# Kernel optimization log

Measured on AMD Instinct MI355X. Metric: run time of the kernel, lower is better.

The kernel has to match this reference:

```python
import jax, jax.numpy as jnp
import numpy as np

N_NODES = 100000
N_EDGES = 3200000
F_IN = 256
HID = 64
N_CLS = 16


def setup_inputs() -> dict:
    key = jax.random.key(0)
    ks = jax.random.split(key, 12)
    x = jax.random.normal(ks[0], (N_NODES, F_IN), dtype=jnp.float32)
    edge_index = jax.random.randint(ks[1], (2, N_EDGES), 0, N_NODES, dtype=jnp.int32)
    w_mul = jax.random.normal(ks[2], (N_EDGES, 1), dtype=jnp.float32)
    s1 = 1.0 / np.sqrt(F_IN)
    s2 = 1.0 / np.sqrt(HID)
    # layer 1 params
    lin1_w = jax.random.uniform(ks[3], (HID, F_IN), minval=-s1, maxval=s1, dtype=jnp.float32)
    lin1_b = jax.random.uniform(ks[4], (HID,), minval=-s1, maxval=s1, dtype=jnp.float32)
    mlp1_w0 = jax.random.uniform(ks[5], (HID, 1), minval=-1.0, maxval=1.0, dtype=jnp.float32)
    mlp1_w1 = jax.random.uniform(ks[6], (HID, HID), minval=-s2, maxval=s2, dtype=jnp.float32)
    mlp1_b1 = jax.random.uniform(ks[7], (HID,), minval=-s2, maxval=s2, dtype=jnp.float32)
    # layer 2 params
    lin2_w = jax.random.uniform(ks[8], (N_CLS, HID), minval=-s2, maxval=s2, dtype=jnp.float32)
    lin2_b = jax.random.uniform(ks[9], (N_CLS,), minval=-s2, maxval=s2, dtype=jnp.float32)
    mlp2_w0 = jax.random.uniform(ks[10], (HID, 1), minval=-1.0, maxval=1.0, dtype=jnp.float32)
    mlp2_w1 = jax.random.uniform(ks[11], (N_CLS, HID), minval=-s2, maxval=s2, dtype=jnp.float32)
    mlp2_b1 = jnp.zeros((N_CLS,), dtype=jnp.float32)
    return dict(x=x, edge_index=edge_index, w_mul=w_mul,
                lin1_w=lin1_w, lin1_b=lin1_b, mlp1_w0=mlp1_w0, mlp1_w1=mlp1_w1, mlp1_b1=mlp1_b1,
                lin2_w=lin2_w, lin2_b=lin2_b, mlp2_w0=mlp2_w0, mlp2_w1=mlp2_w1, mlp2_b1=mlp2_b1)


def curv_layer(x, src, dst, w_mul, lin_w, lin_b, m_w0, m_w1, m_b1, n_nodes):
    # dense projection: [N, out]
    h = x @ lin_w.T + lin_b
    # per-edge weight MLP: Linear(1,HID,no bias) -> LeakyReLU(0.2) -> Linear(HID,out,bias)
    ew = jax.nn.leaky_relu(w_mul @ m_w0.T, negative_slope=0.2) @ m_w1.T + m_b1  # [E, out]
    # segment softmax keyed by source node (PyG softmax(out_weight, edge_index[0]))
    emax = jax.ops.segment_max(ew, src, num_segments=n_nodes)  # [N, out]
    e = jnp.exp(ew - emax[src])
    esum = jax.ops.segment_sum(e, src, num_segments=n_nodes)
    alpha = e / (esum[src] + 1e-16)  # [E, out]
    # message = alpha * x_j (x_j = h[src]); scatter-add at destination
    msg = alpha * h[src]
    return jax.ops.segment_sum(msg, dst, num_segments=n_nodes)  # [N, out]


def reference(x, edge_index, w_mul,
              lin1_w, lin1_b, mlp1_w0, mlp1_w1, mlp1_b1,
              lin2_w, lin2_b, mlp2_w0, mlp2_w1, mlp2_b1):
    src, dst = edge_index[0], edge_index[1]
    n = x.shape[0]
    # eval mode: dropout(p=0.8) is identity
    h = curv_layer(x, src, dst, w_mul, lin1_w, lin1_b, mlp1_w0, mlp1_w1, mlp1_b1, n)
    h = jax.nn.elu(h)
    h = curv_layer(h, src, dst, w_mul, lin2_w, lin2_b, mlp2_w0, mlp2_w1, mlp2_b1, n)
    return jax.nn.log_softmax(h, axis=1)
```

## Files before the change

kernel.cpp:

```cpp
#include <hip/hip_runtime.h>
#include <math.h>

#define FIN 256
#define HID 64
#define NCLS 16
#define BSH 8
#define BWD (1 << BSH)
#define NBKMAX 512
#define CAP 9216
#define CHUNK_S 16384
#define CHUNK_D 8192

__global__ __launch_bounds__(512) void init_kernel(int* gcur_s, int* gcur_d) {
    int tid = threadIdx.x;
    gcur_s[tid] = tid * CAP;
    gcur_d[tid] = tid * CAP;
}

__global__ __launch_bounds__(512) void stage_kernel(const int* __restrict__ ei,
                                                    const float* __restrict__ w,
                                                    int* gcur_s, int* gcur_d,
                                                    unsigned int* st_s, uint2* st_d,
                                                    int E, int nchunk_s) {
    __shared__ int lh[NBKMAX];
    __shared__ int lofs[NBKMAX];
    __shared__ int lcur[NBKMAX];
    __shared__ int gbase[NBKMAX];
    __shared__ uint2 buf2[CHUNK_D];
    unsigned int* buf1 = (unsigned int*)buf2;
    int tid = threadIdx.x;
    int side = (blockIdx.x >= nchunk_s) ? 1 : 0;
    lh[tid] = 0;
    __syncthreads();
    if (!side) {
        int base = blockIdx.x * CHUNK_S;
        #pragma unroll
        for (int j = 0; j < CHUNK_S / 512; j++) {
            int e = base + tid + j * 512;
            if (e < E) atomicAdd(&lh[((unsigned)ei[e]) >> BSH], 1);
        }
    } else {
        int base = (blockIdx.x - nchunk_s) * CHUNK_D;
        #pragma unroll
        for (int j = 0; j < CHUNK_D / 512; j++) {
            int e = base + tid + j * 512;
            if (e < E) atomicAdd(&lh[((unsigned)ei[E + e]) >> BSH], 1);
        }
    }
    __syncthreads();
    int v = lh[tid];
    lofs[tid] = v;
    __syncthreads();
    for (int off = 1; off < 512; off <<= 1) {
        int add = (tid >= off) ? lofs[tid - off] : 0;
        __syncthreads();
        lofs[tid] += add;
        __syncthreads();
    }
    int ex = lofs[tid] - v;
    lofs[tid] = ex;
    lcur[tid] = ex;
    __syncthreads();
    if (!side) {
        int base = blockIdx.x * CHUNK_S;
        #pragma unroll
        for (int j = 0; j < CHUNK_S / 512; j++) {
            int e = base + tid + j * 512;
            if (e < E) {
                int s = ei[e];
                unsigned int rec = (__float_as_uint(w[e]) & 0xFFFFFF00u) | (unsigned int)(s & 0xFF);
                int p = atomicAdd(&lcur[((unsigned)s) >> BSH], 1);
                buf1[p] = rec;
            }
        }
    } else {
        int base = (blockIdx.x - nchunk_s) * CHUNK_D;
        #pragma unroll
        for (int j = 0; j < CHUNK_D / 512; j++) {
            int e = base + tid + j * 512;
            if (e < E) {
                int d = ei[E + e];
                int s = ei[e];
                unsigned int rec = (__float_as_uint(w[e]) & 0xFFFFFF00u) | (unsigned int)(d & 0xFF);
                int p = atomicAdd(&lcur[((unsigned)d) >> BSH], 1);
                buf2[p] = make_uint2((unsigned int)s, rec);
            }
        }
    }
    __syncthreads();
    {
        int c = lh[tid];
        if (c) gbase[tid] = atomicAdd(side ? &gcur_d[tid] : &gcur_s[tid], c);
    }
    __syncthreads();
    int wv = tid >> 6, lane = tid & 63;
    if (!side) {
        for (int b = wv; b < NBKMAX; b += 8) {
            int c = lh[b];
            int ls = lofs[b], gs = gbase[b];
            for (int i = lane; i < c; i += 64) st_s[gs + i] = buf1[ls + i];
        }
    } else {
        for (int b = wv; b < NBKMAX; b += 8) {
            int c = lh[b];
            int ls = lofs[b], gs = gbase[b];
            for (int i = lane; i < c; i += 64) st_d[gs + i] = buf2[ls + i];
        }
    }
}

__global__ __launch_bounds__(512) void bucket_scan_kernel(const int* gcur_s, const int* gcur_d,
                                                          int* bbase_s, int* bbase_d,
                                                          int* offs_s, int* offs_d,
                                                          int N, int nbk, int E) {
    int side = blockIdx.x;
    const int* gc = side ? gcur_d : gcur_s;
    int* bb = side ? bbase_d : bbase_s;
    __shared__ int tmp[512];
    int tid = threadIdx.x;
    int v = (tid < nbk) ? (gc[tid] - tid * CAP) : 0;
    tmp[tid] = v;
    __syncthreads();
    for (int off = 1; off < 512; off <<= 1) {
        int add = (tid >= off) ? tmp[tid - off] : 0;
        __syncthreads();
        tmp[tid] += add;
        __syncthreads();
    }
    if (tid < nbk) bb[tid] = tmp[tid] - v;
    if (tid == 0) {
        bb[nbk] = E;
        (side ? offs_d : offs_s)[N] = E;
    }
}

__global__ __launch_bounds__(256) void bucket_build_s_kernel(const int* __restrict__ bbase,
                                                             const unsigned int* __restrict__ st,
                                                             int* offs, float* t_s, int N) {
    int b = blockIdx.x;
    int r0 = bbase[b];
    int cnt = bbase[b + 1] - r0;
    if (cnt > CAP) cnt = CAP;
    size_t sb = (size_t)b * CAP;
    int n0 = b << BSH;
    int nn = min(BWD, N - n0);
    __shared__ int lh[BWD];
    __shared__ int lofs[BWD];
    __shared__ float buf[CAP];
    int tid = threadIdx.x;
    lh[tid] = 0;
    __syncthreads();
    for (int i = tid; i < cnt; i += 256) atomicAdd(&lh[st[sb + i] & 0xFFu], 1);
    __syncthreads();
    int v = lh[tid];
    lofs[tid] = v;
    __syncthreads();
    for (int off = 1; off < 256; off <<= 1) {
        int add = (tid >= off) ? lofs[tid - off] : 0;
        __syncthreads();
        lofs[tid] += add;
        __syncthreads();
    }
    int ex = lofs[tid] - v;
    if (tid < nn) offs[n0 + tid] = r0 + ex;
    lofs[tid] = ex;
    __syncthreads();
    for (int i = tid; i < cnt; i += 256) {
        unsigned int rec = st[sb + i];
        int p = atomicAdd(&lofs[rec & 0xFFu], 1);
        buf[p] = __uint_as_float(rec & 0xFFFFFF00u);
    }
    __syncthreads();
    for (int i = tid; i < cnt; i += 256) t_s[r0 + i] = buf[i];
}

__global__ __launch_bounds__(256) void bucket_build_d_kernel(const int* __restrict__ bbase,
                                                             const uint2* __restrict__ st,
                                                             int* offs, int2* ed, int N) {
    int b = blockIdx.x;
    int r0 = bbase[b];
    int cnt = bbase[b + 1] - r0;
    if (cnt > CAP) cnt = CAP;
    size_t sb = (size_t)b * CAP;
    int n0 = b << BSH;
    int nn = min(BWD, N - n0);
    __shared__ int lh[BWD];
    __shared__ int lofs[BWD];
    __shared__ int2 buf[CAP];
    int tid = threadIdx.x;
    lh[tid] = 0;
    __syncthreads();
    for (int i = tid; i < cnt; i += 256) atomicAdd(&lh[st[sb + i].y & 0xFFu], 1);
    __syncthreads();
    int v = lh[tid];
    lofs[tid] = v;
    __syncthreads();
    for (int off = 1; off < 256; off <<= 1) {
        int add = (tid >= off) ? lofs[tid - off] : 0;
        __syncthreads();
        lofs[tid] += add;
        __syncthreads();
    }
    int ex = lofs[tid] - v;
    if (tid < nn) offs[n0 + tid] = r0 + ex;
    lofs[tid] = ex;
    __syncthreads();
    for (int i = tid; i < cnt; i += 256) {
        uint2 rec = st[sb + i];
        int p = atomicAdd(&lofs[rec.y & 0xFFu], 1);
        buf[p] = make_int2((int)rec.x, (int)(rec.y & 0xFFFFFF00u));
    }
    __syncthreads();
    for (int i = tid; i < cnt; i += 256) ed[r0 + i] = buf[i];
}

__global__ void prep_kernel(const float* __restrict__ w0a, const float* __restrict__ w1a,
                            const float* __restrict__ w0b, const float* __restrict__ w1b,
                            float* Ap1, float* An1, float* Ap2, float* An2) {
    int tid = threadIdx.x;
    if (tid < 64) {
        float ap = 0.f, an = 0.f;
        for (int j = 0; j < 64; j++) {
            float w0 = w0a[j];
            float w1 = w1a[tid * 64 + j];
            ap += w0 * ((w0 >= 0.f) ? 1.f : 0.2f) * w1;
            an += w0 * ((w0 <= 0.f) ? 1.f : 0.2f) * w1;
        }
        Ap1[tid] = ap; An1[tid] = an;
    } else if (tid < 80) {
        int k = tid - 64;
        float ap = 0.f, an = 0.f;
        for (int j = 0; j < 64; j++) {
            float w0 = w0b[j];
            float w1 = w1b[k * 64 + j];
            ap += w0 * ((w0 >= 0.f) ? 1.f : 0.2f) * w1;
            an += w0 * ((w0 <= 0.f) ? 1.f : 0.2f) * w1;
        }
        Ap2[k] = ap; An2[k] = an;
    }
}

__global__ __launch_bounds__(256) void esum1_kernel(const int* __restrict__ offs,
                                                    const float* __restrict__ t_s,
                                                    const float* __restrict__ Ap,
                                                    const float* __restrict__ An,
                                                    float* __restrict__ inv, int N) {
    int node = blockIdx.x * 4 + (threadIdx.x >> 6);
    int k = threadIdx.x & 63;
    if (node >= N) return;
    int s0 = offs[node], s1 = offs[node + 1];
    float ap = Ap[k], an = An[k];
    float sum = 0.f;
    int i = s0;
    for (; i + 3 < s1; i += 4) {
        float t0 = t_s[i], t1 = t_s[i + 1], t2 = t_s[i + 2], t3 = t_s[i + 3];
        sum += __expf(t0 * ((t0 >= 0.f) ? ap : an));
        sum += __expf(t1 * ((t1 >= 0.f) ? ap : an));
        sum += __expf(t2 * ((t2 >= 0.f) ? ap : an));
        sum += __expf(t3 * ((t3 >= 0.f) ? ap : an));
    }
    for (; i < s1; i++) {
        float t = t_s[i];
        sum += __expf(t * ((t >= 0.f) ? ap : an));
    }
    inv[(size_t)node * 64 + k] = (s1 > s0) ? 1.f / (sum + 1e-16f) : 0.f;
}

__global__ __launch_bounds__(256) void esum2_kernel(const int* __restrict__ offs,
                                                    const float* __restrict__ t_s,
                                                    const float* __restrict__ Ap,
                                                    const float* __restrict__ An,
                                                    float* __restrict__ inv, int N) {
    int node = blockIdx.x * 16 + (threadIdx.x >> 4);
    int k = threadIdx.x & 15;
    if (node >= N) return;
    int s0 = offs[node], s1 = offs[node + 1];
    float ap = Ap[k], an = An[k];
    float sum = 0.f;
    int i = s0;
    for (; i + 3 < s1; i += 4) {
        float t0 = t_s[i], t1 = t_s[i + 1], t2 = t_s[i + 2], t3 = t_s[i + 3];
        sum += __expf(t0 * ((t0 >= 0.f) ? ap : an));
        sum += __expf(t1 * ((t1 >= 0.f) ? ap : an));
        sum += __expf(t2 * ((t2 >= 0.f) ? ap : an));
        sum += __expf(t3 * ((t3 >= 0.f) ? ap : an));
    }
    for (; i < s1; i++) {
        float t = t_s[i];
        sum += __expf(t * ((t >= 0.f) ? ap : an));
    }
    inv[(size_t)node * 16 + k] = (s1 > s0) ? 1.f / (sum + 1e-16f) : 0.f;
}

__device__ __forceinline__ unsigned int bf16rn(float f) {
    unsigned int u = __float_as_uint(f);
    return (u + 0x7fffu + ((u >> 16) & 1u)) >> 16;
}

#define GP 68
__global__ __launch_bounds__(256) void gemm1_kernel(const float* __restrict__ x,
                                                    const float* __restrict__ W,
                                                    const float* __restrict__ b,
                                                    const float* __restrict__ inv,
                                                    uint2* __restrict__ g1, int N) {
    __shared__ float xs[32][GP];
    __shared__ float wsh[32][GP];
    int block_row = blockIdx.x * 64;
    int tid = threadIdx.x;
    int tr = tid / 16, tc = tid % 16;
    float acc[4][4] = {{0.f}};
    for (int k0 = 0; k0 < FIN; k0 += 32) {
        #pragma unroll
        for (int i = 0; i < 2; i++) {
            int idx = tid + i * 256;
            int r = idx >> 3;
            int c4 = idx & 7;
            int gr = block_row + r;
            float4 v = (gr < N) ? *(const float4*)&x[(size_t)gr * FIN + k0 + c4 * 4]
                                : make_float4(0.f, 0.f, 0.f, 0.f);
            xs[c4 * 4 + 0][r] = v.x; xs[c4 * 4 + 1][r] = v.y;
            xs[c4 * 4 + 2][r] = v.z; xs[c4 * 4 + 3][r] = v.w;
            float4 wv = *(const float4*)&W[r * FIN + k0 + c4 * 4];
            wsh[c4 * 4 + 0][r] = wv.x; wsh[c4 * 4 + 1][r] = wv.y;
            wsh[c4 * 4 + 2][r] = wv.z; wsh[c4 * 4 + 3][r] = wv.w;
        }
        __syncthreads();
        #pragma unroll
        for (int kk = 0; kk < 32; kk++) {
            float4 xv = *(const float4*)&xs[kk][tr * 4];
            float4 wv = *(const float4*)&wsh[kk][tc * 4];
            acc[0][0] += xv.x * wv.x; acc[0][1] += xv.x * wv.y; acc[0][2] += xv.x * wv.z; acc[0][3] += xv.x * wv.w;
            acc[1][0] += xv.y * wv.x; acc[1][1] += xv.y * wv.y; acc[1][2] += xv.y * wv.z; acc[1][3] += xv.y * wv.w;
            acc[2][0] += xv.z * wv.x; acc[2][1] += xv.z * wv.y; acc[2][2] += xv.z * wv.z; acc[2][3] += xv.z * wv.w;
            acc[3][0] += xv.w * wv.x; acc[3][1] += xv.w * wv.y; acc[3][2] += xv.w * wv.z; acc[3][3] += xv.w * wv.w;
        }
        __syncthreads();
    }
    float4 bv = ((const float4*)b)[tc];
    #pragma unroll
    for (int i = 0; i < 4; i++) {
        int gr = block_row + tr * 4 + i;
        if (gr < N) {
            float4 iv = *(const float4*)&inv[(size_t)gr * 64 + tc * 4];
            float o0 = (acc[i][0] + bv.x) * iv.x;
            float o1 = (acc[i][1] + bv.y) * iv.y;
            float o2 = (acc[i][2] + bv.z) * iv.z;
            float o3 = (acc[i][3] + bv.w) * iv.w;
            uint2 p;
            p.x = bf16rn(o0) | (bf16rn(o1) << 16);
            p.y = bf16rn(o2) | (bf16rn(o3) << 16);
            g1[(size_t)gr * 16 + tc] = p;
        }
    }
}

__global__ __launch_bounds__(256) void gemm2_kernel(const float* __restrict__ x2,
                                                    const float* __restrict__ W2,
                                                    const float* __restrict__ b2,
                                                    const float* __restrict__ inv,
                                                    float* __restrict__ g2, int N) {
    __shared__ float ws[16][GP];
    __shared__ float xs[16][GP];
    __shared__ float bs[16];
    int tid = threadIdx.x;
    {
        int c = tid >> 4, j4 = tid & 15;
        float4 v = ((const float4*)W2)[tid];
        ws[c][j4 * 4 + 0] = v.x; ws[c][j4 * 4 + 1] = v.y;
        ws[c][j4 * 4 + 2] = v.z; ws[c][j4 * 4 + 3] = v.w;
    }
    if (tid < 16) bs[tid] = b2[tid];
    int node0 = blockIdx.x * 16;
    {
        int r = tid >> 4, c4 = tid & 15;
        int gn = node0 + r;
        float4 v = (gn < N) ? *(const float4*)&x2[(size_t)gn * 64 + c4 * 4]
                            : make_float4(0.f, 0.f, 0.f, 0.f);
        xs[r][c4 * 4 + 0] = v.x; xs[r][c4 * 4 + 1] = v.y;
        xs[r][c4 * 4 + 2] = v.z; xs[r][c4 * 4 + 3] = v.w;
    }
    __syncthreads();
    int node_l = tid >> 4, col = tid & 15;
    int gn = node0 + node_l;
    if (gn >= N) return;
    float acc = bs[col];
    #pragma unroll
    for (int j4 = 0; j4 < 16; j4++) {
        float4 xv = *(const float4*)&xs[node_l][j4 * 4];
        float4 wv = *(const float4*)&ws[col][j4 * 4];
        acc += xv.x * wv.x + xv.y * wv.y + xv.z * wv.z + xv.w * wv.w;
    }
    g2[(size_t)gn * NCLS + col] = acc * inv[(size_t)gn * NCLS + col];
}

__global__ __launch_bounds__(256) void agg1_kernel(const int* __restrict__ offs,
                                                   const int2* __restrict__ ed,
                                                   const float* __restrict__ Ap,
                                                   const float* __restrict__ An,
                                                   const uint2* __restrict__ g,
                                                   float* __restrict__ x2, int N) {
    int node = blockIdx.x * 16 + (threadIdx.x >> 4);
    int l = threadIdx.x & 15;
    if (node >= N) return;
    int d0 = offs[node], d1 = offs[node + 1];
    float4 ap = ((const float4*)Ap)[l];
    float4 an = ((const float4*)An)[l];
    float4 acc = make_float4(0.f, 0.f, 0.f, 0.f);
    int i = d0;
    int end8 = d0 + ((d1 - d0) & ~7);
    for (; i < end8; i += 8) {
        int2 e[8];
        #pragma unroll
        for (int j = 0; j < 8; j++) e[j] = ed[i + j];
        uint2 gv[8];
        #pragma unroll
        for (int j = 0; j < 8; j++)
            gv[j] = g[((size_t)e[j].x << 4) + l];
        #pragma unroll
        for (int j = 0; j < 8; j++) {
            float t = __int_as_float(e[j].y);
            float4 a = (t >= 0.f) ? ap : an;
            float ex = __expf(t * a.x), ey = __expf(t * a.y);
            float ez = __expf(t * a.z), ew = __expf(t * a.w);
            acc.x += ex * __uint_as_float(gv[j].x << 16);
            acc.y += ey * __uint_as_float(gv[j].x & 0xffff0000u);
            acc.z += ez * __uint_as_float(gv[j].y << 16);
            acc.w += ew * __uint_as_float(gv[j].y & 0xffff0000u);
        }
    }
    for (; i < d1; i++) {
        int2 e = ed[i];
        float t = __int_as_float(e.y);
        float4 a = (t >= 0.f) ? ap : an;
        uint2 gv = g[((size_t)e.x << 4) + l];
        acc.x += __expf(t * a.x) * __uint_as_float(gv.x << 16);
        acc.y += __expf(t * a.y) * __uint_as_float(gv.x & 0xffff0000u);
        acc.z += __expf(t * a.z) * __uint_as_float(gv.y << 16);
        acc.w += __expf(t * a.w) * __uint_as_float(gv.y & 0xffff0000u);
    }
    float4 o;
    o.x = (acc.x > 0.f) ? acc.x : (__expf(acc.x) - 1.f);
    o.y = (acc.y > 0.f) ? acc.y : (__expf(acc.y) - 1.f);
    o.z = (acc.z > 0.f) ? acc.z : (__expf(acc.z) - 1.f);
    o.w = (acc.w > 0.f) ? acc.w : (__expf(acc.w) - 1.f);
    *(float4*)(x2 + ((size_t)node << 6) + l * 4) = o;
}

__global__ __launch_bounds__(256) void agg2_kernel(const int* __restrict__ offs,
                                                   const int2* __restrict__ ed,
                                                   const float* __restrict__ Ap,
                                                   const float* __restrict__ An,
                                                   const float* __restrict__ g,
                                                   float* __restrict__ out, int N) {
    int node = blockIdx.x * 64 + (threadIdx.x >> 2);
    int l = threadIdx.x & 3;
    if (node >= N) return;
    int d0 = offs[node], d1 = offs[node + 1];
    float4 ap = ((const float4*)Ap)[l];
    float4 an = ((const float4*)An)[l];
    float4 acc = make_float4(0.f, 0.f, 0.f, 0.f);
    int i = d0;
    int end8 = d0 + ((d1 - d0) & ~7);
    for (; i < end8; i += 8) {
        int2 e[8];
        #pragma unroll
        for (int j = 0; j < 8; j++) e[j] = ed[i + j];
        float4 gv[8];
        #pragma unroll
        for (int j = 0; j < 8; j++)
            gv[j] = *(const float4*)(g + ((size_t)e[j].x << 4) + l * 4);
        #pragma unroll
        for (int j = 0; j < 8; j++) {
            float t = __int_as_float(e[j].y);
            float4 a = (t >= 0.f) ? ap : an;
            acc.x += __expf(t * a.x) * gv[j].x;
            acc.y += __expf(t * a.y) * gv[j].y;
            acc.z += __expf(t * a.z) * gv[j].z;
            acc.w += __expf(t * a.w) * gv[j].w;
        }
    }
    for (; i < d1; i++) {
        int2 e = ed[i];
        float t = __int_as_float(e.y);
        float4 a = (t >= 0.f) ? ap : an;
        float4 gv = *(const float4*)(g + ((size_t)e.x << 4) + l * 4);
        acc.x += __expf(t * a.x) * gv.x;
        acc.y += __expf(t * a.y) * gv.y;
        acc.z += __expf(t * a.z) * gv.z;
        acc.w += __expf(t * a.w) * gv.w;
    }
    float m = fmaxf(fmaxf(acc.x, acc.y), fmaxf(acc.z, acc.w));
    m = fmaxf(m, __shfl_xor(m, 1, 4));
    m = fmaxf(m, __shfl_xor(m, 2, 4));
    float s = __expf(acc.x - m) + __expf(acc.y - m) + __expf(acc.z - m) + __expf(acc.w - m);
    s += __shfl_xor(s, 1, 4);
    s += __shfl_xor(s, 2, 4);
    float lse = m + __logf(s);
    float4 o = make_float4(acc.x - lse, acc.y - lse, acc.z - lse, acc.w - lse);
    *(float4*)(out + ((size_t)node << 4) + l * 4) = o;
}

extern "C" void kernel_launch(void* const* d_in, const int* in_sizes, int n_in,
                              void* d_out, int out_size, void* d_ws, size_t ws_size,
                              hipStream_t stream) {
    const float* x      = (const float*)d_in[0];
    const int*   ei     = (const int*)d_in[1];
    const float* wmul   = (const float*)d_in[2];
    const float* lin1_w = (const float*)d_in[3];
    const float* lin1_b = (const float*)d_in[4];
    const float* m1w0   = (const float*)d_in[5];
    const float* m1w1   = (const float*)d_in[6];
    const float* lin2_w = (const float*)d_in[8];
    const float* lin2_b = (const float*)d_in[9];
    const float* m2w0   = (const float*)d_in[10];
    const float* m2w1   = (const float*)d_in[11];

    int N = in_sizes[0] / FIN;
    int E = in_sizes[1] / 2;
    int nbk = (N + BWD - 1) >> BSH;
    int nchunk_s = (E + CHUNK_S - 1) / CHUNK_S;
    int nchunk_d = (E + CHUNK_D - 1) / CHUNK_D;

    char* ws = (char*)d_ws;
    auto alloc = [&](size_t bytes) {
        char* p = ws;
        ws += (bytes + 255) & ~(size_t)255;
        return p;
    };
    int*   gcur_s  = (int*)alloc(NBKMAX * 4);
    int*   gcur_d  = (int*)alloc(NBKMAX * 4);
    int*   bbase_s = (int*)alloc((NBKMAX + 1) * 4);
    int*   bbase_d = (int*)alloc((NBKMAX + 1) * 4);
    float* Ap1     = (float*)alloc(64 * 4);
    float* An1     = (float*)alloc(64 * 4);
    float* Ap2     = (float*)alloc(16 * 4);
    float* An2     = (float*)alloc(16 * 4);
    int*   offs_s  = (int*)alloc((size_t)(N + 1) * 4);
    int*   offs_d  = (int*)alloc((size_t)(N + 1) * 4);
    float* t_s     = (float*)alloc((size_t)E * 4);
    int2*  ed      = (int2*)alloc((size_t)E * 8);
    char*  reg = ws;
    unsigned int* st_s = (unsigned int*)(reg);
    uint2*        st_d = (uint2*)(reg + (((size_t)nbk * CAP * 4 + 255) & ~(size_t)255));
    float* inv1 = (float*)(reg);
    float* x2   = (float*)(reg);
    char*  regB = reg + (((size_t)N * 64 * 4 + 255) & ~(size_t)255);
    uint2* g1   = (uint2*)(regB);
    float* inv2 = (float*)(regB + ((size_t)N * 16 * 8));
    float* g2   = (float*)(regB + ((size_t)N * 16 * 8) + ((size_t)N * 16 * 4));

    init_kernel<<<1, 512, 0, stream>>>(gcur_s, gcur_d);
    prep_kernel<<<1, 128, 0, stream>>>(m1w0, m1w1, m2w0, m2w1, Ap1, An1, Ap2, An2);
    stage_kernel<<<nchunk_s + nchunk_d, 512, 0, stream>>>(ei, wmul, gcur_s, gcur_d,
                                                          st_s, st_d, E, nchunk_s);
    bucket_scan_kernel<<<2, 512, 0, stream>>>(gcur_s, gcur_d, bbase_s, bbase_d,
                                              offs_s, offs_d, N, nbk, E);
    bucket_build_s_kernel<<<nbk, 256, 0, stream>>>(bbase_s, st_s, offs_s, t_s, N);
    bucket_build_d_kernel<<<nbk, 256, 0, stream>>>(bbase_d, st_d, offs_d, ed, N);
    esum1_kernel<<<(N + 3) / 4, 256, 0, stream>>>(offs_s, t_s, Ap1, An1, inv1, N);
    gemm1_kernel<<<(N + 63) / 64, 256, 0, stream>>>(x, lin1_w, lin1_b, inv1, g1, N);
    agg1_kernel<<<(N + 15) / 16, 256, 0, stream>>>(offs_d, ed, Ap1, An1, g1, x2, N);
    esum2_kernel<<<(N + 15) / 16, 256, 0, stream>>>(offs_s, t_s, Ap2, An2, inv2, N);
    gemm2_kernel<<<(N + 15) / 16, 256, 0, stream>>>(x2, lin2_w, lin2_b, inv2, g2, N);
    agg2_kernel<<<(N + 63) / 64, 256, 0, stream>>>(offs_d, ed, Ap2, An2, g2, (float*)d_out, N);
}
```

Measured before the change: 527.0 us.

## Partition each node's edges by sign of weight and use exp2 with prescaled coefficients

The bucket build kernels now sort each node's edges into two sub-segments, one for non-negative edge weights and one for negative, and record a per-node midpoint array. The esum and aggregation kernels loop over each half with a fixed coefficient vector, so the per-edge select between the positive and negative coefficients goes away. The coefficients are also prescaled by log2(e) in prep, so the loops can call the hardware exp2 directly. This adds two N-sized midpoint arrays, a larger shared histogram, and a second loop tail per node.

```diff
diff --git a/kernel.cpp b/kernel.cpp
--- a/kernel.cpp
+++ b/kernel.cpp
@@ -136,7 +136,7 @@
 
 __global__ __launch_bounds__(256) void bucket_build_s_kernel(const int* __restrict__ bbase,
                                                              const unsigned int* __restrict__ st,
-                                                             int* offs, float* t_s, int N) {
+                                                             int* offs, int* mid, float* t_s, int N) {
     int b = blockIdx.x;
     int r0 = bbase[b];
     int cnt = bbase[b + 1] - r0;
@@ -144,30 +144,40 @@
     size_t sb = (size_t)b * CAP;
     int n0 = b << BSH;
     int nn = min(BWD, N - n0);
-    __shared__ int lh[BWD];
-    __shared__ int lofs[BWD];
+    __shared__ int lh[2 * BWD];
+    __shared__ int lscan[BWD];
+    __shared__ int lcur[2 * BWD];
     __shared__ float buf[CAP];
     int tid = threadIdx.x;
     lh[tid] = 0;
-    __syncthreads();
-    for (int i = tid; i < cnt; i += 256) atomicAdd(&lh[st[sb + i] & 0xFFu], 1);
-    __syncthreads();
-    int v = lh[tid];
-    lofs[tid] = v;
-    __syncthreads();
-    for (int off = 1; off < 256; off <<= 1) {
-        int add = (tid >= off) ? lofs[tid - off] : 0;
-        __syncthreads();
-        lofs[tid] += add;
-        __syncthreads();
-    }
-    int ex = lofs[tid] - v;
-    if (tid < nn) offs[n0 + tid] = r0 + ex;
-    lofs[tid] = ex;
+    lh[tid + BWD] = 0;
     __syncthreads();
     for (int i = tid; i < cnt; i += 256) {
         unsigned int rec = st[sb + i];
-        int p = atomicAdd(&lofs[rec & 0xFFu], 1);
+        atomicAdd(&lh[((rec & 0xFFu) << 1) | (rec >> 31)], 1);
+    }
+    __syncthreads();
+    int c0 = lh[2 * tid], c1 = lh[2 * tid + 1];
+    int v = c0 + c1;
+    lscan[tid] = v;
+    __syncthreads();
+    for (int off = 1; off < 256; off <<= 1) {
+        int add = (tid >= off) ? lscan[tid - off] : 0;
+        __syncthreads();
+        lscan[tid] += add;
+        __syncthreads();
+    }
+    int ex = lscan[tid] - v;
+    if (tid < nn) {
+        offs[n0 + tid] = r0 + ex;
+        mid[n0 + tid] = r0 + ex + c0;
+    }
+    lcur[2 * tid] = ex;
+    lcur[2 * tid + 1] = ex + c0;
+    __syncthreads();
+    for (int i = tid; i < cnt; i += 256) {
+        unsigned int rec = st[sb + i];
+        int p = atomicAdd(&lcur[((rec & 0xFFu) << 1) | (rec >> 31)], 1);
         buf[p] = __uint_as_float(rec & 0xFFFFFF00u);
     }
     __syncthreads();
@@ -176,7 +186,7 @@
 
 __global__ __launch_bounds__(256) void bucket_build_d_kernel(const int* __restrict__ bbase,
                                                              const uint2* __restrict__ st,
-                                                             int* offs, int2* ed, int N) {
+                                                             int* offs, int* mid, int2* ed, int N) {
     int b = blockIdx.x;
     int r0 = bbase[b];
     int cnt = bbase[b + 1] - r0;
@@ -184,36 +194,47 @@
     size_t sb = (size_t)b * CAP;
     int n0 = b << BSH;
     int nn = min(BWD, N - n0);
-    __shared__ int lh[BWD];
-    __shared__ int lofs[BWD];
+    __shared__ int lh[2 * BWD];
+    __shared__ int lscan[BWD];
+    __shared__ int lcur[2 * BWD];
     __shared__ int2 buf[CAP];
     int tid = threadIdx.x;
     lh[tid] = 0;
-    __syncthreads();
-    for (int i = tid; i < cnt; i += 256) atomicAdd(&lh[st[sb + i].y & 0xFFu], 1);
-    __syncthreads();
-    int v = lh[tid];
-    lofs[tid] = v;
+    lh[tid + BWD] = 0;
+    __syncthreads();
+    for (int i = tid; i < cnt; i += 256) {
+        unsigned int ry = st[sb + i].y;
+        atomicAdd(&lh[((ry & 0xFFu) << 1) | (ry >> 31)], 1);
+    }
+    __syncthreads();
+    int c0 = lh[2 * tid], c1 = lh[2 * tid + 1];
+    int v = c0 + c1;
+    lscan[tid] = v;
     __syncthreads();
     for (int off = 1; off < 256; off <<= 1) {
-        int add = (tid >= off) ? lofs[tid - off] : 0;
-        __syncthreads();
-        lofs[tid] += add;
-        __syncthreads();
-    }
-    int ex = lofs[tid] - v;
-    if (tid < nn) offs[n0 + tid] = r0 + ex;
-    lofs[tid] = ex;
+        int add = (tid >= off) ? lscan[tid - off] : 0;
+        __syncthreads();
+        lscan[tid] += add;
+        __syncthreads();
+    }
+    int ex = lscan[tid] - v;
+    if (tid < nn) {
+        offs[n0 + tid] = r0 + ex;
+        mid[n0 + tid] = r0 + ex + c0;
+    }
+    lcur[2 * tid] = ex;
+    lcur[2 * tid + 1] = ex + c0;
     __syncthreads();
     for (int i = tid; i < cnt; i += 256) {
         uint2 rec = st[sb + i];
-        int p = atomicAdd(&lofs[rec.y & 0xFFu], 1);
+        int p = atomicAdd(&lcur[((rec.y & 0xFFu) << 1) | (rec.y >> 31)], 1);
         buf[p] = make_int2((int)rec.x, (int)(rec.y & 0xFFFFFF00u));
     }
     __syncthreads();
     for (int i = tid; i < cnt; i += 256) ed[r0 + i] = buf[i];
 }
 
+#define LOG2E 1.44269504088896340736f
 __global__ void prep_kernel(const float* __restrict__ w0a, const float* __restrict__ w1a,
                             const float* __restrict__ w0b, const float* __restrict__ w1b,
                             float* Ap1, float* An1, float* Ap2, float* An2) {
@@ -226,7 +247,7 @@
             ap += w0 * ((w0 >= 0.f) ? 1.f : 0.2f) * w1;
             an += w0 * ((w0 <= 0.f) ? 1.f : 0.2f) * w1;
         }
-        Ap1[tid] = ap; An1[tid] = an;
+        Ap1[tid] = ap * LOG2E; An1[tid] = an * LOG2E;
     } else if (tid < 80) {
         int k = tid - 64;
         float ap = 0.f, an = 0.f;
@@ -236,11 +257,26 @@
             ap += w0 * ((w0 >= 0.f) ? 1.f : 0.2f) * w1;
             an += w0 * ((w0 <= 0.f) ? 1.f : 0.2f) * w1;
         }
-        Ap2[k] = ap; An2[k] = an;
-    }
+        Ap2[k] = ap * LOG2E; An2[k] = an * LOG2E;
+    }
+}
+
+__device__ __forceinline__ float seg_expsum(const float* __restrict__ t, int i0, int i1, float a) {
+    float sum = 0.f;
+    int i = i0;
+    for (; i + 3 < i1; i += 4) {
+        float t0 = t[i], t1 = t[i + 1], t2 = t[i + 2], t3 = t[i + 3];
+        sum += __builtin_amdgcn_exp2f(t0 * a);
+        sum += __builtin_amdgcn_exp2f(t1 * a);
+        sum += __builtin_amdgcn_exp2f(t2 * a);
+        sum += __builtin_amdgcn_exp2f(t3 * a);
+    }
+    for (; i < i1; i++) sum += __builtin_amdgcn_exp2f(t[i] * a);
+    return sum;
 }
 
 __global__ __launch_bounds__(256) void esum1_kernel(const int* __restrict__ offs,
+                                                    const int* __restrict__ mid,
                                                     const float* __restrict__ t_s,
                                                     const float* __restrict__ Ap,
                                                     const float* __restrict__ An,
@@ -248,25 +284,13 @@
     int node = blockIdx.x * 4 + (threadIdx.x >> 6);
     int k = threadIdx.x & 63;
     if (node >= N) return;
-    int s0 = offs[node], s1 = offs[node + 1];
-    float ap = Ap[k], an = An[k];
-    float sum = 0.f;
-    int i = s0;
-    for (; i + 3 < s1; i += 4) {
-        float t0 = t_s[i], t1 = t_s[i + 1], t2 = t_s[i + 2], t3 = t_s[i + 3];
-        sum += __expf(t0 * ((t0 >= 0.f) ? ap : an));
-        sum += __expf(t1 * ((t1 >= 0.f) ? ap : an));
-        sum += __expf(t2 * ((t2 >= 0.f) ? ap : an));
-        sum += __expf(t3 * ((t3 >= 0.f) ? ap : an));
-    }
-    for (; i < s1; i++) {
-        float t = t_s[i];
-        sum += __expf(t * ((t >= 0.f) ? ap : an));
-    }
+    int s0 = offs[node], m = mid[node], s1 = offs[node + 1];
+    float sum = seg_expsum(t_s, s0, m, Ap[k]) + seg_expsum(t_s, m, s1, An[k]);
     inv[(size_t)node * 64 + k] = (s1 > s0) ? 1.f / (sum + 1e-16f) : 0.f;
 }
 
 __global__ __launch_bounds__(256) void esum2_kernel(const int* __restrict__ offs,
+                                                    const int* __restrict__ mid,
                                                     const float* __restrict__ t_s,
                                                     const float* __restrict__ Ap,
                                                     const float* __restrict__ An,
@@ -274,21 +298,8 @@
     int node = blockIdx.x * 16 + (threadIdx.x >> 4);
     int k = threadIdx.x & 15;
     if (node >= N) return;
-    int s0 = offs[node], s1 = offs[node + 1];
-    float ap = Ap[k], an = An[k];
-    float sum = 0.f;
-    int i = s0;
-    for (; i + 3 < s1; i += 4) {
-        float t0 = t_s[i], t1 = t_s[i + 1], t2 = t_s[i + 2], t3 = t_s[i + 3];
-        sum += __expf(t0 * ((t0 >= 0.f) ? ap : an));
-        sum += __expf(t1 * ((t1 >= 0.f) ? ap : an));
-        sum += __expf(t2 * ((t2 >= 0.f) ? ap : an));
-        sum += __expf(t3 * ((t3 >= 0.f) ? ap : an));
-    }
-    for (; i < s1; i++) {
-        float t = t_s[i];
-        sum += __expf(t * ((t >= 0.f) ? ap : an));
-    }
+    int s0 = offs[node], m = mid[node], s1 = offs[node + 1];
+    float sum = seg_expsum(t_s, s0, m, Ap[k]) + seg_expsum(t_s, m, s1, An[k]);
     inv[(size_t)node * 16 + k] = (s1 > s0) ? 1.f / (sum + 1e-16f) : 0.f;
 }
 
@@ -393,7 +404,41 @@
     g2[(size_t)gn * NCLS + col] = acc * inv[(size_t)gn * NCLS + col];
 }
 
+__device__ __forceinline__ void agg1_half(const int2* __restrict__ ed,
+                                          const uint2* __restrict__ g,
+                                          int i0, int i1, int l, float4 a, float4& acc) {
+    int i = i0;
+    int end8 = i0 + ((i1 - i0) & ~7);
+    for (; i < end8; i += 8) {
+        int2 e[8];
+        #pragma unroll
+        for (int j = 0; j < 8; j++) e[j] = ed[i + j];
+        uint2 gv[8];
+        #pragma unroll
+        for (int j = 0; j < 8; j++)
+            gv[j] = g[((size_t)e[j].x << 4) + l];
+        #pragma unroll
+        for (int j = 0; j < 8; j++) {
+            float t = __int_as_float(e[j].y);
+            acc.x += __builtin_amdgcn_exp2f(t * a.x) * __uint_as_float(gv[j].x << 16);
+            acc.y += __builtin_amdgcn_exp2f(t * a.y) * __uint_as_float(gv[j].x & 0xffff0000u);
+            acc.z += __builtin_amdgcn_exp2f(t * a.z) * __uint_as_float(gv[j].y << 16);
+            acc.w += __builtin_amdgcn_exp2f(t * a.w) * __uint_as_float(gv[j].y & 0xffff0000u);
+        }
+    }
+    for (; i < i1; i++) {
+        int2 e = ed[i];
+        float t = __int_as_float(e.y);
+        uint2 gv = g[((size_t)e.x << 4) + l];
+        acc.x += __builtin_amdgcn_exp2f(t * a.x) * __uint_as_float(gv.x << 16);
+        acc.y += __builtin_amdgcn_exp2f(t * a.y) * __uint_as_float(gv.x & 0xffff0000u);
+        acc.z += __builtin_amdgcn_exp2f(t * a.z) * __uint_as_float(gv.y << 16);
+        acc.w += __builtin_amdgcn_exp2f(t * a.w) * __uint_as_float(gv.y & 0xffff0000u);
+    }
+}
+
 __global__ __launch_bounds__(256) void agg1_kernel(const int* __restrict__ offs,
+                                                   const int* __restrict__ mid,
                                                    const int2* __restrict__ ed,
                                                    const float* __restrict__ Ap,
                                                    const float* __restrict__ An,
@@ -402,42 +447,12 @@
     int node = blockIdx.x * 16 + (threadIdx.x >> 4);
     int l = threadIdx.x & 15;
     if (node >= N) return;
-    int d0 = offs[node], d1 = offs[node + 1];
+    int d0 = offs[node], m = mid[node], d1 = offs[node + 1];
     float4 ap = ((const float4*)Ap)[l];
     float4 an = ((const float4*)An)[l];
     float4 acc = make_float4(0.f, 0.f, 0.f, 0.f);
-    int i = d0;
-    int end8 = d0 + ((d1 - d0) & ~7);
-    for (; i < end8; i += 8) {
-        int2 e[8];
-        #pragma unroll
-        for (int j = 0; j < 8; j++) e[j] = ed[i + j];
-        uint2 gv[8];
-        #pragma unroll
-        for (int j = 0; j < 8; j++)
-            gv[j] = g[((size_t)e[j].x << 4) + l];
-        #pragma unroll
-        for (int j = 0; j < 8; j++) {
-            float t = __int_as_float(e[j].y);
-            float4 a = (t >= 0.f) ? ap : an;
-            float ex = __expf(t * a.x), ey = __expf(t * a.y);
-            float ez = __expf(t * a.z), ew = __expf(t * a.w);
-            acc.x += ex * __uint_as_float(gv[j].x << 16);
-            acc.y += ey * __uint_as_float(gv[j].x & 0xffff0000u);
-            acc.z += ez * __uint_as_float(gv[j].y << 16);
-            acc.w += ew * __uint_as_float(gv[j].y & 0xffff0000u);
-        }
-    }
-    for (; i < d1; i++) {
-        int2 e = ed[i];
-        float t = __int_as_float(e.y);
-        float4 a = (t >= 0.f) ? ap : an;
-        uint2 gv = g[((size_t)e.x << 4) + l];
-        acc.x += __expf(t * a.x) * __uint_as_float(gv.x << 16);
-        acc.y += __expf(t * a.y) * __uint_as_float(gv.x & 0xffff0000u);
-        acc.z += __expf(t * a.z) * __uint_as_float(gv.y << 16);
-        acc.w += __expf(t * a.w) * __uint_as_float(gv.y & 0xffff0000u);
-    }
+    agg1_half(ed, g, d0, m, l, ap, acc);
+    agg1_half(ed, g, m, d1, l, an, acc);
     float4 o;
     o.x = (acc.x > 0.f) ? acc.x : (__expf(acc.x) - 1.f);
     o.y = (acc.y > 0.f) ? acc.y : (__expf(acc.y) - 1.f);
@@ -446,7 +461,41 @@
     *(float4*)(x2 + ((size_t)node << 6) + l * 4) = o;
 }
 
+__device__ __forceinline__ void agg2_half(const int2* __restrict__ ed,
+                                          const float* __restrict__ g,
+                                          int i0, int i1, int l, float4 a, float4& acc) {
+    int i = i0;
+    int end8 = i0 + ((i1 - i0) & ~7);
+    for (; i < end8; i += 8) {
+        int2 e[8];
+        #pragma unroll
+        for (int j = 0; j < 8; j++) e[j] = ed[i + j];
+        float4 gv[8];
+        #pragma unroll
+        for (int j = 0; j < 8; j++)
+            gv[j] = *(const float4*)(g + ((size_t)e[j].x << 4) + l * 4);
+        #pragma unroll
+        for (int j = 0; j < 8; j++) {
+            float t = __int_as_float(e[j].y);
+            acc.x += __builtin_amdgcn_exp2f(t * a.x) * gv[j].x;
+            acc.y += __builtin_amdgcn_exp2f(t * a.y) * gv[j].y;
+            acc.z += __builtin_amdgcn_exp2f(t * a.z) * gv[j].z;
+            acc.w += __builtin_amdgcn_exp2f(t * a.w) * gv[j].w;
+        }
+    }
+    for (; i < i1; i++) {
+        int2 e = ed[i];
+        float t = __int_as_float(e.y);
+        float4 gv = *(const float4*)(g + ((size_t)e.x << 4) + l * 4);
+        acc.x += __builtin_amdgcn_exp2f(t * a.x) * gv.x;
+        acc.y += __builtin_amdgcn_exp2f(t * a.y) * gv.y;
+        acc.z += __builtin_amdgcn_exp2f(t * a.z) * gv.z;
+        acc.w += __builtin_amdgcn_exp2f(t * a.w) * gv.w;
+    }
+}
+
 __global__ __launch_bounds__(256) void agg2_kernel(const int* __restrict__ offs,
+                                                   const int* __restrict__ mid,
                                                    const int2* __restrict__ ed,
                                                    const float* __restrict__ Ap,
                                                    const float* __restrict__ An,
@@ -455,47 +504,19 @@
     int node = blockIdx.x * 64 + (threadIdx.x >> 2);
     int l = threadIdx.x & 3;
     if (node >= N) return;
-    int d0 = offs[node], d1 = offs[node + 1];
+    int d0 = offs[node], m = mid[node], d1 = offs[node + 1];
     float4 ap = ((const float4*)Ap)[l];
     float4 an = ((const float4*)An)[l];
     float4 acc = make_float4(0.f, 0.f, 0.f, 0.f);
-    int i = d0;
-    int end8 = d0 + ((d1 - d0) & ~7);
-    for (; i < end8; i += 8) {
-        int2 e[8];
-        #pragma unroll
-        for (int j = 0; j < 8; j++) e[j] = ed[i + j];
-        float4 gv[8];
-        #pragma unroll
-        for (int j = 0; j < 8; j++)
-            gv[j] = *(const float4*)(g + ((size_t)e[j].x << 4) + l * 4);
-        #pragma unroll
-        for (int j = 0; j < 8; j++) {
-            float t = __int_as_float(e[j].y);
-            float4 a = (t >= 0.f) ? ap : an;
-            acc.x += __expf(t * a.x) * gv[j].x;
-            acc.y += __expf(t * a.y) * gv[j].y;
-            acc.z += __expf(t * a.z) * gv[j].z;
-            acc.w += __expf(t * a.w) * gv[j].w;
-        }
-    }
-    for (; i < d1; i++) {
-        int2 e = ed[i];
-        float t = __int_as_float(e.y);
-        float4 a = (t >= 0.f) ? ap : an;
-        float4 gv = *(const float4*)(g + ((size_t)e.x << 4) + l * 4);
-        acc.x += __expf(t * a.x) * gv.x;
-        acc.y += __expf(t * a.y) * gv.y;
-        acc.z += __expf(t * a.z) * gv.z;
-        acc.w += __expf(t * a.w) * gv.w;
-    }
-    float m = fmaxf(fmaxf(acc.x, acc.y), fmaxf(acc.z, acc.w));
-    m = fmaxf(m, __shfl_xor(m, 1, 4));
-    m = fmaxf(m, __shfl_xor(m, 2, 4));
-    float s = __expf(acc.x - m) + __expf(acc.y - m) + __expf(acc.z - m) + __expf(acc.w - m);
+    agg2_half(ed, g, d0, m, l, ap, acc);
+    agg2_half(ed, g, m, d1, l, an, acc);
+    float mx = fmaxf(fmaxf(acc.x, acc.y), fmaxf(acc.z, acc.w));
+    mx = fmaxf(mx, __shfl_xor(mx, 1, 4));
+    mx = fmaxf(mx, __shfl_xor(mx, 2, 4));
+    float s = __expf(acc.x - mx) + __expf(acc.y - mx) + __expf(acc.z - mx) + __expf(acc.w - mx);
     s += __shfl_xor(s, 1, 4);
     s += __shfl_xor(s, 2, 4);
-    float lse = m + __logf(s);
+    float lse = mx + __logf(s);
     float4 o = make_float4(acc.x - lse, acc.y - lse, acc.z - lse, acc.w - lse);
     *(float4*)(out + ((size_t)node << 4) + l * 4) = o;
 }
@@ -537,6 +558,8 @@
     float* An2     = (float*)alloc(16 * 4);
     int*   offs_s  = (int*)alloc((size_t)(N + 1) * 4);
     int*   offs_d  = (int*)alloc((size_t)(N + 1) * 4);
+    int*   mid_s   = (int*)alloc((size_t)N * 4);
+    int*   mid_d   = (int*)alloc((size_t)N * 4);
     float* t_s     = (float*)alloc((size_t)E * 4);
     int2*  ed      = (int2*)alloc((size_t)E * 8);
     char*  reg = ws;
@@ -555,12 +578,12 @@
                                                           st_s, st_d, E, nchunk_s);
     bucket_scan_kernel<<<2, 512, 0, stream>>>(gcur_s, gcur_d, bbase_s, bbase_d,
                                               offs_s, offs_d, N, nbk, E);
-    bucket_build_s_kernel<<<nbk, 256, 0, stream>>>(bbase_s, st_s, offs_s, t_s, N);
-    bucket_build_d_kernel<<<nbk, 256, 0, stream>>>(bbase_d, st_d, offs_d, ed, N);
-    esum1_kernel<<<(N + 3) / 4, 256, 0, stream>>>(offs_s, t_s, Ap1, An1, inv1, N);
+    bucket_build_s_kernel<<<nbk, 256, 0, stream>>>(bbase_s, st_s, offs_s, mid_s, t_s, N);
+    bucket_build_d_kernel<<<nbk, 256, 0, stream>>>(bbase_d, st_d, offs_d, mid_d, ed, N);
+    esum1_kernel<<<(N + 3) / 4, 256, 0, stream>>>(offs_s, mid_s, t_s, Ap1, An1, inv1, N);
     gemm1_kernel<<<(N + 63) / 64, 256, 0, stream>>>(x, lin1_w, lin1_b, inv1, g1, N);
-    agg1_kernel<<<(N + 15) / 16, 256, 0, stream>>>(offs_d, ed, Ap1, An1, g1, x2, N);
-    esum2_kernel<<<(N + 15) / 16, 256, 0, stream>>>(offs_s, t_s, Ap2, An2, inv2, N);
+    agg1_kernel<<<(N + 15) / 16, 256, 0, stream>>>(offs_d, mid_d, ed, Ap1, An1, g1, x2, N);
+    esum2_kernel<<<(N + 15) / 16, 256, 0, stream>>>(offs_s, mid_s, t_s, Ap2, An2, inv2, N);
     gemm2_kernel<<<(N + 15) / 16, 256, 0, stream>>>(x2, lin2_w, lin2_b, inv2, g2, N);
-    agg2_kernel<<<(N + 63) / 64, 256, 0, stream>>>(offs_d, ed, Ap2, An2, g2, (float*)d_out, N);
-}
+    agg2_kernel<<<(N + 63) / 64, 256, 0, stream>>>(offs_d, mid_d, ed, Ap2, An2, g2, (float*)d_out, N);
+}
```

After: 542.5 us. 3.0% more time.
